# Optimization experiments

Measured on AMD Instinct MI355X. Metric: run time of the kernel, lower is better.

Reference implementation:

```python
import jax, jax.numpy as jnp
import numpy as np

MIDC = 128
HEADS = 8
HEADC = MIDC // HEADS
EPS = 1e-5


def setup_inputs() -> dict:
    key = jax.random.key(0)
    ks = jax.random.split(key, 8)
    B, C, H, W = 8, MIDC, 256, 256
    s = 1.0 / np.sqrt(C)
    x = jax.random.normal(ks[0], (B, C, H, W), dtype=jnp.float32)
    qkv_w = jax.random.normal(ks[1], (3 * C, C), dtype=jnp.float32) * s
    o1_w = jax.random.normal(ks[2], (C, C), dtype=jnp.float32) * s
    o2_w = jax.random.normal(ks[3], (C, C), dtype=jnp.float32) * s
    kln_w = 1.0 + 0.1 * jax.random.normal(ks[4], (HEADS, 1, HEADC), dtype=jnp.float32)
    kln_b = 0.1 * jax.random.normal(ks[5], (HEADS, 1, HEADC), dtype=jnp.float32)
    vln_w = 1.0 + 0.1 * jax.random.normal(ks[6], (HEADS, 1, HEADC), dtype=jnp.float32)
    vln_b = 0.1 * jax.random.normal(ks[7], (HEADS, 1, HEADC), dtype=jnp.float32)
    return {"x": x, "qkv_w": qkv_w, "o1_w": o1_w, "o2_w": o2_w,
            "kln_w": kln_w, "kln_b": kln_b, "vln_w": vln_w, "vln_b": vln_b}


def _ln(t, w, b):
    # torch LayerNorm variant: unbiased std, eps added to std (not variance)
    m = t.mean(-1, keepdims=True)
    s = jnp.std(t, axis=-1, ddof=1, keepdims=True)
    return w * ((t - m) / (s + EPS)) + b


def reference(x, qkv_w, o1_w, o2_w, kln_w, kln_b, vln_w, vln_b):
    B, C, H, W = x.shape
    hc = C // HEADS
    N = H * W
    # 1x1 conv == pointwise matmul over channel dim
    qkv = jnp.einsum('oc,bchw->bhwo', qkv_w, x)            # (B,H,W,3C)
    qkv = qkv.reshape(B, N, HEADS, 3 * hc).transpose(0, 2, 1, 3)  # (B,heads,N,3hc)
    q, k, v = jnp.split(qkv, 3, axis=-1)
    k = _ln(k, kln_w, kln_b)
    v = _ln(v, vln_w, vln_b)
    kv = jnp.einsum('bhnd,bhne->bhde', k, v) / N            # (B,heads,hc,hc)
    o = jnp.einsum('bhnd,bhde->bhne', q, kv)                # (B,heads,N,hc)
    o = o.transpose(0, 2, 1, 3).reshape(B, H, W, C).transpose(0, 3, 1, 2)
    ret = o + x
    u = jnp.einsum('oc,bchw->bohw', o1_w, ret)
    u = jax.nn.gelu(u, approximate=False)
    u = jnp.einsum('oc,bchw->bohw', o2_w, u) + x
    return jax.nn.gelu(u, approximate=False)
```

## Files before the change

kernel.cpp:

```cpp
#include <hip/hip_runtime.h>

#define EPS 1e-5f

typedef _Float16 half8_t __attribute__((ext_vector_type(8)));
typedef _Float16 half4_t __attribute__((ext_vector_type(4)));
typedef float    float4_t __attribute__((ext_vector_type(4)));

__device__ __forceinline__ float gelu_f(float v) {
  float u2 = v * v;
  float a  = __builtin_fmaf(u2, -0.10294322f, -2.3022078f);
  float e  = __builtin_amdgcn_exp2f(v * a);
  return v * __builtin_amdgcn_rcpf(1.0f + e);
}

template<int CTRL>
__device__ __forceinline__ float dpp_add(float v) {
  int j = __builtin_amdgcn_update_dpp(0, __float_as_int(v), CTRL, 0xF, 0xF, true);
  return v + __int_as_float(j);
}
__device__ __forceinline__ float rsum16(float v) {
  v = dpp_add<0xB1>(v);
  v = dpp_add<0x4E>(v);
  v = dpp_add<0x124>(v);
  v = dpp_add<0x128>(v);
  return v;
}

__global__ __launch_bounds__(256)
void k_wconv(const float* __restrict__ qkvw, const float* __restrict__ o1w,
             const float* __restrict__ o2w, _Float16* __restrict__ kvw,
             _Float16* __restrict__ qw, _Float16* __restrict__ o1h,
             _Float16* __restrict__ o2h) {
  int t = blockIdx.x * 256 + threadIdx.x;
  if (t < 32768) {
    int r = t >> 7, c = t & 127;
    int h = r >> 5, rr = r & 31;
    int src = h * 48 + 16 + rr;
    int mb  = h * 48 + 16 + (rr & 16);
    float s = 0.0f;
#pragma unroll
    for (int d = 0; d < 16; d++) s += qkvw[(mb + d) * 128 + c];
    kvw[t] = (_Float16)(qkvw[src * 128 + c] - 0.0625f * s);
  } else if (t < 49152) {
    int i = t - 32768;
    int r = i >> 7, c = i & 127;
    int src = (r >> 4) * 48 + (r & 15);
    qw[i] = (_Float16)qkvw[src * 128 + c];
  } else if (t < 65536) {
    int i = t - 49152;
    o1h[i] = (_Float16)o1w[i];
  } else {
    int i = t - 65536;
    o2h[i] = (_Float16)o2w[i];
  }
}

__global__ __launch_bounds__(256, 5)
void k_qkv_kv(const float* __restrict__ x, const _Float16* __restrict__ kvw,
              const float* __restrict__ klw, const float* __restrict__ klb,
              const float* __restrict__ vlw, const float* __restrict__ vlb,
              float* __restrict__ partial) {
  __shared__ _Float16 xs[64][136];
  const int t = threadIdx.x;
  const int lane = t & 63, w = t >> 6;
  const int quad = lane >> 4, l16 = lane & 15;
  const int b = blockIdx.x >> 8, cb = blockIdx.x & 255;
  const float* xb = x + (long)b * 8388608;

  float kw0[2], kb0[2], vw0[2], vb0[2];
#pragma unroll
  for (int hh = 0; hh < 2; hh++) {
    int h = 2 * w + hh;
    kw0[hh] = klw[h * 16 + l16]; kb0[hh] = klb[h * 16 + l16];
    vw0[hh] = vlw[h * 16 + l16]; vb0[hh] = vlb[h * 16 + l16];
  }

  float4_t kvacc[2] = {};

  for (int ch = 0; ch < 4; ch++) {
    const int n0 = cb * 256 + ch * 64;
#pragma unroll
    for (int i = 0; i < 8; i++) {
      int f = i * 256 + t;
      int c = f >> 4, pg = f & 15;
      float4 v = *(const float4*)(xb + ((long)c << 16) + n0 + 4 * pg);
      xs[4 * pg + 0][c] = (_Float16)v.x;
      xs[4 * pg + 1][c] = (_Float16)v.y;
      xs[4 * pg + 2][c] = (_Float16)v.z;
      xs[4 * pg + 3][c] = (_Float16)v.w;
    }
    __syncthreads();

    float4_t acc[4][4] = {};
#pragma unroll
    for (int k = 0; k < 4; k++) {
      half8_t A[4];
#pragma unroll
      for (int mt = 0; mt < 4; mt++)
        A[mt] = *(const half8_t*)&xs[mt * 16 + l16][k * 32 + quad * 8];
#pragma unroll
      for (int ot = 0; ot < 4; ot++) {
        half8_t Bf = *(const half8_t*)(kvw + (w * 64 + ot * 16 + l16) * 128 + k * 32 + quad * 8);
#pragma unroll
        for (int mt = 0; mt < 4; mt++)
          acc[mt][ot] = __builtin_amdgcn_mfma_f32_16x16x32_f16(A[mt], Bf, acc[mt][ot], 0, 0, 0);
      }
    }

#pragma unroll
    for (int hh = 0; hh < 2; hh++) {
#pragma unroll
      for (int mt = 0; mt < 4; mt++) {
        half4_t kf, vf;
#pragma unroll
        for (int rr = 0; rr < 4; rr++) {
          float kx = acc[mt][2 * hh + 0][rr];
          float vx = acc[mt][2 * hh + 1][rr];
          float s2k = rsum16(kx * kx);
          float s2v = rsum16(vx * vx);
          float rk = __builtin_amdgcn_rcpf(
              __builtin_fmaf(__builtin_amdgcn_sqrtf(s2k), 0.25819889f, EPS));
          float rv = __builtin_amdgcn_rcpf(
              __builtin_fmaf(__builtin_amdgcn_sqrtf(s2v), 0.25819889f, EPS));
          kf[rr] = (_Float16)((kw0[hh] * rk) * kx + kb0[hh]);
          vf[rr] = (_Float16)((vw0[hh] * rv) * vx + vb0[hh]);
        }
        kvacc[hh] = __builtin_amdgcn_mfma_f32_16x16x16f16(kf, vf, kvacc[hh], 0, 0, 0);
      }
    }
    __syncthreads();
  }

#pragma unroll
  for (int hh = 0; hh < 2; hh++) {
    int h = 2 * w + hh;
#pragma unroll
    for (int rr = 0; rr < 4; rr++) {
      int d = quad * 4 + rr;
      partial[((long)blockIdx.x * 8 + h) * 256 + d * 16 + l16] = kvacc[hh][rr];
    }
  }
}

__global__ __launch_bounds__(256)
void k_reduce(const float* __restrict__ partial, float* __restrict__ kvT) {
  const int bh = blockIdx.x;
  const int t = threadIdx.x;
  const int b = bh >> 3, h = bh & 7;
  float s = 0.0f;
#pragma unroll 8
  for (int cb = 0; cb < 256; cb++)
    s += partial[((long)(b * 256 + cb) * 8 + h) * 256 + t];
  kvT[(bh << 8) + (t & 15) * 16 + (t >> 4)] = s * (1.0f / 65536.0f);
}

__device__ __forceinline__ void gemm_128(const _Float16* src, const _Float16* wgt,
                                         int w, int l16, int quad, float4_t (&acc)[4][2]) {
#pragma unroll
  for (int k = 0; k < 4; k++) {
    half8_t A[4];
#pragma unroll
    for (int mt = 0; mt < 4; mt++)
      A[mt] = *(const half8_t*)(src + (mt * 16 + l16) * 136 + k * 32 + quad * 8);
#pragma unroll
    for (int ot = 0; ot < 2; ot++) {
      half8_t Bf = *(const half8_t*)(wgt + (w * 32 + ot * 16 + l16) * 128 + k * 32 + quad * 8);
#pragma unroll
      for (int mt = 0; mt < 4; mt++)
        acc[mt][ot] = __builtin_amdgcn_mfma_f32_16x16x32_f16(A[mt], Bf, acc[mt][ot], 0, 0, 0);
    }
  }
}

__global__ __launch_bounds__(256, 4)
void k_attn_out(const float* __restrict__ x, const _Float16* __restrict__ qw,
                const _Float16* __restrict__ o1h, const _Float16* __restrict__ o2h,
                const float* __restrict__ kvT, float* __restrict__ out) {
  __shared__ _Float16 bufA[64][136];
  __shared__ _Float16 bufB[64][136];
  const int t = threadIdx.x;
  const int lane = t & 63, w = t >> 6;
  const int quad = lane >> 4, l16 = lane & 15;
  const int b = blockIdx.x >> 10;
  const int n0 = (blockIdx.x & 1023) << 6;
  const float* xb = x + (long)b * 8388608;

#pragma unroll
  for (int i = 0; i < 8; i++) {
    int f = i * 256 + t, c = f >> 4, pg = f & 15;
    float4 v = *(const float4*)(xb + ((long)c << 16) + n0 + 4 * pg);
    bufA[4 * pg + 0][c] = (_Float16)v.x;
    bufA[4 * pg + 1][c] = (_Float16)v.y;
    bufA[4 * pg + 2][c] = (_Float16)v.z;
    bufA[4 * pg + 3][c] = (_Float16)v.w;
  }

  half4_t kvf[2];
#pragma unroll
  for (int hh = 0; hh < 2; hh++) {
    int h = 2 * w + hh;
    float4 kq = *(const float4*)(kvT + ((b * 8 + h) << 8) + l16 * 16 + quad * 4);
    kvf[hh][0] = (_Float16)kq.x; kvf[hh][1] = (_Float16)kq.y;
    kvf[hh][2] = (_Float16)kq.z; kvf[hh][3] = (_Float16)kq.w;
  }
  __syncthreads();

  float4_t qa[4][2] = {};
  gemm_128(&bufA[0][0], qw, w, l16, quad, qa);
#pragma unroll
  for (int mt = 0; mt < 4; mt++)
#pragma unroll
    for (int ot = 0; ot < 2; ot++)
#pragma unroll
      for (int rr = 0; rr < 4; rr++)
        bufB[mt * 16 + quad * 4 + rr][w * 32 + ot * 16 + l16] = (_Float16)qa[mt][ot][rr];

#pragma unroll
  for (int hh = 0; hh < 2; hh++) {
    int h = 2 * w + hh;
#pragma unroll
    for (int mt = 0; mt < 4; mt++) {
      half4_t qf = *(const half4_t*)&bufB[mt * 16 + l16][h * 16 + quad * 4];
      float4_t oacc = {};
      oacc = __builtin_amdgcn_mfma_f32_16x16x16f16(qf, kvf[hh], oacc, 0, 0, 0);
#pragma unroll
      for (int rr = 0; rr < 4; rr++) {
        int p = mt * 16 + quad * 4 + rr, c = h * 16 + l16;
        bufB[p][c] = (_Float16)(oacc[rr] + (float)bufA[p][c]);
      }
    }
  }

  _Float16 xres[4][2][4];
#pragma unroll
  for (int mt = 0; mt < 4; mt++)
#pragma unroll
    for (int ot = 0; ot < 2; ot++)
#pragma unroll
      for (int rr = 0; rr < 4; rr++)
        xres[mt][ot][rr] = bufA[mt * 16 + quad * 4 + rr][w * 32 + ot * 16 + l16];
  __syncthreads();

  float4_t ua[4][2] = {};
  gemm_128(&bufB[0][0], o1h, w, l16, quad, ua);
#pragma unroll
  for (int mt = 0; mt < 4; mt++)
#pragma unroll
    for (int ot = 0; ot < 2; ot++)
#pragma unroll
      for (int rr = 0; rr < 4; rr++)
        bufA[mt * 16 + quad * 4 + rr][w * 32 + ot * 16 + l16] = (_Float16)gelu_f(ua[mt][ot][rr]);
  __syncthreads();

  float4_t ya[4][2] = {};
  gemm_128(&bufA[0][0], o2h, w, l16, quad, ya);
#pragma unroll
  for (int mt = 0; mt < 4; mt++)
#pragma unroll
    for (int ot = 0; ot < 2; ot++)
#pragma unroll
      for (int rr = 0; rr < 4; rr++) {
        int p = mt * 16 + quad * 4 + rr, c = w * 32 + ot * 16 + l16;
        bufB[p][c] = (_Float16)gelu_f(ya[mt][ot][rr] + (float)xres[mt][ot][rr]);
      }
  __syncthreads();

#pragma unroll
  for (int i = 0; i < 8; i++) {
    int f = i * 256 + t, c = f >> 4, pg = f & 15;
    float4 o4;
    o4.x = (float)bufB[4 * pg + 0][c];
    o4.y = (float)bufB[4 * pg + 1][c];
    o4.z = (float)bufB[4 * pg + 2][c];
    o4.w = (float)bufB[4 * pg + 3][c];
    *(float4*)(out + ((long)b * 128 + c) * 65536 + n0 + 4 * pg) = o4;
  }
}

extern "C" void kernel_launch(void* const* d_in, const int* in_sizes, int n_in,
                              void* d_out, int out_size, void* d_ws, size_t ws_size,
                              hipStream_t stream) {
  const float* x    = (const float*)d_in[0];
  const float* qkvw = (const float*)d_in[1];
  const float* o1w  = (const float*)d_in[2];
  const float* o2w  = (const float*)d_in[3];
  const float* klw  = (const float*)d_in[4];
  const float* klb  = (const float*)d_in[5];
  const float* vlw  = (const float*)d_in[6];
  const float* vlb  = (const float*)d_in[7];
  float* out = (float*)d_out;
  char* ws = (char*)d_ws;
  _Float16* kvw  = (_Float16*)(ws + 0);
  _Float16* qw   = (_Float16*)(ws + 65536);
  _Float16* o1h  = (_Float16*)(ws + 98304);
  _Float16* o2h  = (_Float16*)(ws + 131072);
  float* kvT     = (float*)(ws + 163840);
  float* partial = (float*)(ws + 229376);

  k_wconv<<<320, 256, 0, stream>>>(qkvw, o1w, o2w, kvw, qw, o1h, o2h);
  k_qkv_kv<<<2048, 256, 0, stream>>>(x, kvw, klw, klb, vlw, vlb, partial);
  k_reduce<<<64, 256, 0, stream>>>(partial, kvT);
  k_attn_out<<<8192, 256, 0, stream>>>(x, qw, o1h, o2h, kvT, out);
}
```

Before: 889.4 us.

## Swizzle LDS tiles and double-buffer register prefetch in QKV kernel

Replaces the padded LDS tiles with unpadded 128-wide tiles using an XOR swizzle on 8-element column groups in both kernels. The goal is to cut bank conflicts on the transposing scalar stores and on the vector fragment reads. The QKV/KV kernel also double-buffers its shared tile, prefetching the next chunk's global loads into registers in two halves around the MFMA work, and drops the trailing barrier. In exchange it uses more registers and LDS per block, so the occupancy hint falls from 5 to 3 blocks.

```diff
diff --git a/kernel.cpp b/kernel.cpp
--- a/kernel.cpp
+++ b/kernel.cpp
@@ -11,6 +11,15 @@
   float a  = __builtin_fmaf(u2, -0.10294322f, -2.3022078f);
   float e  = __builtin_amdgcn_exp2f(v * a);
   return v * __builtin_amdgcn_rcpf(1.0f + e);
+}
+
+__device__ __forceinline__ int swz(int p, int c) {
+  int g = (p + (p >> 2)) & 15;
+  return (((c >> 3) ^ g) << 3) | (c & 7);
+}
+__device__ __forceinline__ int swz8(int p, int cg) {
+  int g = (p + (p >> 2)) & 15;
+  return (cg ^ g) << 3;
 }
 
 template<int CTRL>
@@ -55,17 +64,18 @@
   }
 }
 
-__global__ __launch_bounds__(256, 5)
+__global__ __launch_bounds__(256, 3)
 void k_qkv_kv(const float* __restrict__ x, const _Float16* __restrict__ kvw,
               const float* __restrict__ klw, const float* __restrict__ klb,
               const float* __restrict__ vlw, const float* __restrict__ vlb,
               float* __restrict__ partial) {
-  __shared__ _Float16 xs[64][136];
+  __shared__ _Float16 xs[2][8192];
   const int t = threadIdx.x;
   const int lane = t & 63, w = t >> 6;
   const int quad = lane >> 4, l16 = lane & 15;
   const int b = blockIdx.x >> 8, cb = blockIdx.x & 255;
   const float* xb = x + (long)b * 8388608;
+  const int cbase = t >> 4, pg = t & 15, p0 = 4 * pg;
 
   float kw0[2], kb0[2], vw0[2], vb0[2];
 #pragma unroll
@@ -76,28 +86,40 @@
   }
 
   float4_t kvacc[2] = {};
+  float4 ld[8];
+
+#pragma unroll
+  for (int i = 0; i < 8; i++)
+    ld[i] = *(const float4*)(xb + ((long)(i * 16 + cbase) << 16) + cb * 256 + p0);
 
   for (int ch = 0; ch < 4; ch++) {
-    const int n0 = cb * 256 + ch * 64;
+    _Float16* bs = xs[ch & 1];
 #pragma unroll
     for (int i = 0; i < 8; i++) {
-      int f = i * 256 + t;
-      int c = f >> 4, pg = f & 15;
-      float4 v = *(const float4*)(xb + ((long)c << 16) + n0 + 4 * pg);
-      xs[4 * pg + 0][c] = (_Float16)v.x;
-      xs[4 * pg + 1][c] = (_Float16)v.y;
-      xs[4 * pg + 2][c] = (_Float16)v.z;
-      xs[4 * pg + 3][c] = (_Float16)v.w;
+      int c = i * 16 + cbase;
+      bs[(p0 + 0) * 128 + swz(p0 + 0, c)] = (_Float16)ld[i].x;
+      bs[(p0 + 1) * 128 + swz(p0 + 1, c)] = (_Float16)ld[i].y;
+      bs[(p0 + 2) * 128 + swz(p0 + 2, c)] = (_Float16)ld[i].z;
+      bs[(p0 + 3) * 128 + swz(p0 + 3, c)] = (_Float16)ld[i].w;
     }
     __syncthreads();
+
+    const int n1 = cb * 256 + (ch + 1) * 64;
+    if (ch < 3) {
+#pragma unroll
+      for (int i = 0; i < 4; i++)
+        ld[i] = *(const float4*)(xb + ((long)(i * 16 + cbase) << 16) + n1 + p0);
+    }
 
     float4_t acc[4][4] = {};
 #pragma unroll
     for (int k = 0; k < 4; k++) {
       half8_t A[4];
 #pragma unroll
-      for (int mt = 0; mt < 4; mt++)
-        A[mt] = *(const half8_t*)&xs[mt * 16 + l16][k * 32 + quad * 8];
+      for (int mt = 0; mt < 4; mt++) {
+        int row = mt * 16 + l16;
+        A[mt] = *(const half8_t*)(bs + row * 128 + swz8(row, k * 4 + quad));
+      }
 #pragma unroll
       for (int ot = 0; ot < 4; ot++) {
         half8_t Bf = *(const half8_t*)(kvw + (w * 64 + ot * 16 + l16) * 128 + k * 32 + quad * 8);
@@ -105,6 +127,12 @@
         for (int mt = 0; mt < 4; mt++)
           acc[mt][ot] = __builtin_amdgcn_mfma_f32_16x16x32_f16(A[mt], Bf, acc[mt][ot], 0, 0, 0);
       }
+    }
+
+    if (ch < 3) {
+#pragma unroll
+      for (int i = 4; i < 8; i++)
+        ld[i] = *(const float4*)(xb + ((long)(i * 16 + cbase) << 16) + n1 + p0);
     }
 
 #pragma unroll
@@ -128,7 +156,6 @@
         kvacc[hh] = __builtin_amdgcn_mfma_f32_16x16x16f16(kf, vf, kvacc[hh], 0, 0, 0);
       }
     }
-    __syncthreads();
   }
 
 #pragma unroll
@@ -160,8 +187,10 @@
   for (int k = 0; k < 4; k++) {
     half8_t A[4];
 #pragma unroll
-    for (int mt = 0; mt < 4; mt++)
-      A[mt] = *(const half8_t*)(src + (mt * 16 + l16) * 136 + k * 32 + quad * 8);
+    for (int mt = 0; mt < 4; mt++) {
+      int row = mt * 16 + l16;
+      A[mt] = *(const half8_t*)(src + row * 128 + swz8(row, k * 4 + quad));
+    }
 #pragma unroll
     for (int ot = 0; ot < 2; ot++) {
       half8_t Bf = *(const half8_t*)(wgt + (w * 32 + ot * 16 + l16) * 128 + k * 32 + quad * 8);
@@ -176,23 +205,24 @@
 void k_attn_out(const float* __restrict__ x, const _Float16* __restrict__ qw,
                 const _Float16* __restrict__ o1h, const _Float16* __restrict__ o2h,
                 const float* __restrict__ kvT, float* __restrict__ out) {
-  __shared__ _Float16 bufA[64][136];
-  __shared__ _Float16 bufB[64][136];
+  __shared__ _Float16 bufA[8192];
+  __shared__ _Float16 bufB[8192];
   const int t = threadIdx.x;
   const int lane = t & 63, w = t >> 6;
   const int quad = lane >> 4, l16 = lane & 15;
   const int b = blockIdx.x >> 10;
   const int n0 = (blockIdx.x & 1023) << 6;
   const float* xb = x + (long)b * 8388608;
+  const int cbase = t >> 4, pg = t & 15, p0 = 4 * pg;
 
 #pragma unroll
   for (int i = 0; i < 8; i++) {
-    int f = i * 256 + t, c = f >> 4, pg = f & 15;
-    float4 v = *(const float4*)(xb + ((long)c << 16) + n0 + 4 * pg);
-    bufA[4 * pg + 0][c] = (_Float16)v.x;
-    bufA[4 * pg + 1][c] = (_Float16)v.y;
-    bufA[4 * pg + 2][c] = (_Float16)v.z;
-    bufA[4 * pg + 3][c] = (_Float16)v.w;
+    int c = i * 16 + cbase;
+    float4 v = *(const float4*)(xb + ((long)c << 16) + n0 + p0);
+    bufA[(p0 + 0) * 128 + swz(p0 + 0, c)] = (_Float16)v.x;
+    bufA[(p0 + 1) * 128 + swz(p0 + 1, c)] = (_Float16)v.y;
+    bufA[(p0 + 2) * 128 + swz(p0 + 2, c)] = (_Float16)v.z;
+    bufA[(p0 + 3) * 128 + swz(p0 + 3, c)] = (_Float16)v.w;
   }
 
   half4_t kvf[2];
@@ -206,27 +236,30 @@
   __syncthreads();
 
   float4_t qa[4][2] = {};
-  gemm_128(&bufA[0][0], qw, w, l16, quad, qa);
+  gemm_128(bufA, qw, w, l16, quad, qa);
 #pragma unroll
   for (int mt = 0; mt < 4; mt++)
 #pragma unroll
     for (int ot = 0; ot < 2; ot++)
 #pragma unroll
-      for (int rr = 0; rr < 4; rr++)
-        bufB[mt * 16 + quad * 4 + rr][w * 32 + ot * 16 + l16] = (_Float16)qa[mt][ot][rr];
+      for (int rr = 0; rr < 4; rr++) {
+        int p = mt * 16 + quad * 4 + rr, c = w * 32 + ot * 16 + l16;
+        bufB[p * 128 + swz(p, c)] = (_Float16)qa[mt][ot][rr];
+      }
 
 #pragma unroll
   for (int hh = 0; hh < 2; hh++) {
     int h = 2 * w + hh;
 #pragma unroll
     for (int mt = 0; mt < 4; mt++) {
-      half4_t qf = *(const half4_t*)&bufB[mt * 16 + l16][h * 16 + quad * 4];
+      int row = mt * 16 + l16;
+      half4_t qf = *(const half4_t*)(bufB + row * 128 + swz(row, h * 16 + quad * 4));
       float4_t oacc = {};
       oacc = __builtin_amdgcn_mfma_f32_16x16x16f16(qf, kvf[hh], oacc, 0, 0, 0);
 #pragma unroll
       for (int rr = 0; rr < 4; rr++) {
         int p = mt * 16 + quad * 4 + rr, c = h * 16 + l16;
-        bufB[p][c] = (_Float16)(oacc[rr] + (float)bufA[p][c]);
+        bufB[p * 128 + swz(p, c)] = (_Float16)(oacc[rr] + (float)bufA[p * 128 + swz(p, c)]);
       }
     }
   }
@@ -237,23 +270,27 @@
 #pragma unroll
     for (int ot = 0; ot < 2; ot++)
 #pragma unroll
-      for (int rr = 0; rr < 4; rr++)
-        xres[mt][ot][rr] = bufA[mt * 16 + quad * 4 + rr][w * 32 + ot * 16 + l16];
+      for (int rr = 0; rr < 4; rr++) {
+        int p = mt * 16 + quad * 4 + rr, c = w * 32 + ot * 16 + l16;
+        xres[mt][ot][rr] = bufA[p * 128 + swz(p, c)];
+      }
   __syncthreads();
 
   float4_t ua[4][2] = {};
-  gemm_128(&bufB[0][0], o1h, w, l16, quad, ua);
+  gemm_128(bufB, o1h, w, l16, quad, ua);
 #pragma unroll
   for (int mt = 0; mt < 4; mt++)
 #pragma unroll
     for (int ot = 0; ot < 2; ot++)
 #pragma unroll
-      for (int rr = 0; rr < 4; rr++)
-        bufA[mt * 16 + quad * 4 + rr][w * 32 + ot * 16 + l16] = (_Float16)gelu_f(ua[mt][ot][rr]);
+      for (int rr = 0; rr < 4; rr++) {
+        int p = mt * 16 + quad * 4 + rr, c = w * 32 + ot * 16 + l16;
+        bufA[p * 128 + swz(p, c)] = (_Float16)gelu_f(ua[mt][ot][rr]);
+      }
   __syncthreads();
 
   float4_t ya[4][2] = {};
-  gemm_128(&bufA[0][0], o2h, w, l16, quad, ya);
+  gemm_128(bufA, o2h, w, l16, quad, ya);
 #pragma unroll
   for (int mt = 0; mt < 4; mt++)
 #pragma unroll
@@ -261,19 +298,19 @@
 #pragma unroll
       for (int rr = 0; rr < 4; rr++) {
         int p = mt * 16 + quad * 4 + rr, c = w * 32 + ot * 16 + l16;
-        bufB[p][c] = (_Float16)gelu_f(ya[mt][ot][rr] + (float)xres[mt][ot][rr]);
+        bufB[p * 128 + swz(p, c)] = (_Float16)gelu_f(ya[mt][ot][rr] + (float)xres[mt][ot][rr]);
       }
   __syncthreads();
 
 #pragma unroll
   for (int i = 0; i < 8; i++) {
-    int f = i * 256 + t, c = f >> 4, pg = f & 15;
+    int c = i * 16 + cbase;
     float4 o4;
-    o4.x = (float)bufB[4 * pg + 0][c];
-    o4.y = (float)bufB[4 * pg + 1][c];
-    o4.z = (float)bufB[4 * pg + 2][c];
-    o4.w = (float)bufB[4 * pg + 3][c];
-    *(float4*)(out + ((long)b * 128 + c) * 65536 + n0 + 4 * pg) = o4;
+    o4.x = (float)bufB[(p0 + 0) * 128 + swz(p0 + 0, c)];
+    o4.y = (float)bufB[(p0 + 1) * 128 + swz(p0 + 1, c)];
+    o4.z = (float)bufB[(p0 + 2) * 128 + swz(p0 + 2, c)];
+    o4.w = (float)bufB[(p0 + 3) * 128 + swz(p0 + 3, c)];
+    *(float4*)(out + ((long)b * 128 + c) * 65536 + n0 + p0) = o4;
   }
 }
 
```

Measured after the change: 1.371 ms. 1.54x slower.
